# Optimization experiments

Measured on AMD Instinct MI355X. Metric: run time of the kernel, lower is better.

The kernel has to match this reference:

```python
import jax, jax.numpy as jnp
import numpy as np

N_NODES = 128
F = 64            # hidden channels (64x0e + 64x1o)
N_RBF = 8
H_R = 64          # radial MLP hidden
L = 2             # num_interactions
R_MAX = 5.0
AVG_NEIGH = 127.0
G_DIM = 16
N_SPECIES = 5

# static fully-connected edge list (no self edges): E = n*(n-1)
_idx = np.arange(N_NODES)
_s, _r = np.meshgrid(_idx, _idx, indexing='ij')
_mask = _s != _r
SENDERS = jnp.asarray(_s[_mask])    # [E]
RECEIVERS = jnp.asarray(_r[_mask])  # [E]


def setup_inputs() -> dict:
    key = jax.random.key(0)
    ks = jax.random.split(key, 12)
    inp = {
        'positions': jax.random.normal(ks[0], (32, N_NODES, 3), jnp.float32),
        'node_features': jax.random.randint(ks[1], (32, N_NODES), 0, N_SPECIES),
        'global_features': jax.random.normal(ks[2], (32, G_DIM), jnp.float32),
        # learned parameters
        'embed': jax.random.normal(ks[3], (N_SPECIES, F), jnp.float32) * 0.1,
        'glob_w': jax.random.normal(ks[4], (G_DIM, F), jnp.float32) * 0.1,
        'rbf_w1': jax.random.normal(ks[5], (L, N_RBF, H_R), jnp.float32) * 0.3,
        'rbf_b1': jnp.zeros((L, H_R), jnp.float32),
        'rbf_w2': jax.random.normal(ks[6], (L, H_R, 3 * F), jnp.float32) * 0.1,
        'ws': jax.random.normal(ks[7], (L, F, F), jnp.float32) * 0.1,
        'wv': jax.random.normal(ks[8], (L, F, F), jnp.float32) * 0.1,
        'wout': jax.random.normal(ks[9], (F,), jnp.float32) * 0.1,
        'final_scaling': jnp.ones((), jnp.float32),
    }
    return inp


def _rbf(d):
    # gaussian radial basis on [0, r_max]
    centers = jnp.linspace(0.0, R_MAX, N_RBF)
    width = R_MAX / N_RBF
    return jnp.exp(-((d[:, None] - centers) ** 2) / (2.0 * width * width))  # [E, N_RBF]


def _single(pos, species, glob, embed, glob_w, rbf_w1, rbf_b1, rbf_w2, ws, wv, wout, final_scaling):
    # graph construction + edge vectors
    edge_vec = pos[RECEIVERS] - pos[SENDERS]                 # [E,3]
    d = jnp.sqrt(jnp.sum(edge_vec ** 2, axis=-1) + 1e-12)   # [E]
    unit = edge_vec / d[:, None]                             # [E,3]
    phi = _rbf(d)                                            # [E,N_RBF]

    # node embedding (species one-hot lookup) conditioned on global features
    s = embed[species] + glob @ glob_w                       # [n,F] scalars
    v = jnp.zeros((N_NODES, F, 3), pos.dtype)                # [n,F,3] vectors

    for l in range(L):
        rw = jax.nn.silu(phi @ rbf_w1[l] + rbf_b1[l]) @ rbf_w2[l]  # [E,3F]
        r1, r2, r3 = jnp.split(rw, 3, axis=-1)               # each [E,F]
        ms = r1 * s[SENDERS]                                 # [E,F]
        mv = r2[..., None] * v[SENDERS] + (r3 * s[SENDERS])[..., None] * unit[:, None, :]  # [E,F,3]
        agg_s = jax.ops.segment_sum(ms, RECEIVERS, num_segments=N_NODES) / AVG_NEIGH
        agg_v = jax.ops.segment_sum(mv, RECEIVERS, num_segments=N_NODES) / AVG_NEIGH
        s = s + agg_s @ ws[l]
        v = v + jnp.einsum('nfd,fg->ngd', agg_v, wv[l])

    out = jnp.einsum('nfd,f->nd', v, wout)                   # equivariant readout [n,3]
    return (out - pos) * final_scaling


def reference(positions, node_features, global_features, embed, glob_w, rbf_w1,
              rbf_b1, rbf_w2, ws, wv, wout, final_scaling):
    fn = lambda p, sp, g: _single(p, sp, g, embed, glob_w, rbf_w1, rbf_b1,
                                  rbf_w2, ws, wv, wout, final_scaling)
    return jax.vmap(fn)(positions, node_features, global_features)
```

## Files before the change

### kernel.cpp

```cpp
#include <hip/hip_runtime.h>
#include <hip/hip_bf16.h>


#define NN 128
#define BB 32
#define FF 64

using f32x4  = __attribute__((ext_vector_type(4))) float;
using short8 = __attribute__((ext_vector_type(8))) short;
using half4  = __attribute__((ext_vector_type(4))) _Float16;

__device__ __forceinline__ unsigned short f2bf(float x) {
    unsigned int u = __float_as_uint(x);
    u += 0x7fff + ((u >> 16) & 1);
    return (unsigned short)(u >> 16);
}
__device__ __forceinline__ unsigned int f2bf_fast32(float x) {
    return (__float_as_uint(x) + 0x8000u) >> 16;
}

__global__ __launch_bounds__(256) void setup_kernel(
    const float* __restrict__ w2,
    const float* __restrict__ ws,
    const float* __restrict__ wv,
    const float* __restrict__ rbf_w1,
    const float* __restrict__ rbf_b1,
    const int* __restrict__ species, const float* __restrict__ glob,
    const float* __restrict__ embed, const float* __restrict__ glob_w,
    short* __restrict__ w2frag,
    float* __restrict__ wT4,
    _Float16* __restrict__ w1A,
    float* __restrict__ s)
{
    const int blk = blockIdx.x;
    if (blk < 192) {
        const int tid = blk * 256 + threadIdx.x;
        const int NFRAG = 24576;
        if (tid < NFRAG) {
            const int e  = tid & 7;
            const int l  = (tid >> 3) & 63;
            const int ks = (tid >> 9) & 1;
            const int q  = tid >> 10;
            const int nt = q % 3;
            const int wv_ = (q / 3) & 3;
            const int layer = q / 12;
            const int col = nt * 64 + wv_ * 16 + (l & 15);
            const int hb  = ks * 32 + (l >> 4) * 8 + e;
            const float val = w2[layer * 64 * 192 + hb * 192 + col] * (1.0f / 127.0f);
            w2frag[tid] = (short)f2bf(val);
        }
        const int tid2 = tid - NFRAG;
        if (tid2 >= 0 && tid2 < 16384) {
            const int c   = tid2 & 3;
            const int g   = (tid2 >> 2) & 63;
            const int ff4 = (tid2 >> 8) & 15;
            const int m   = (tid2 >> 12) & 1;
            const int layer = tid2 >> 13;
            const float* src = (m == 0 ? ws : wv) + layer * 4096;
            wT4[tid2] = src[(ff4 * 4 + c) * 64 + g];
        }
        const int tid3 = tid - NFRAG - 16384;
        if (tid3 >= 0 && tid3 < 2048) {
            const int e  = tid3 & 3;
            const int l  = (tid3 >> 2) & 63;
            const int wv_ = (tid3 >> 8) & 3;
            const int layer = tid3 >> 10;
            const int k = (l >> 4) * 4 + e;
            const int h = wv_ * 16 + (l & 15);
            float val = 0.0f;
            if (k < 8)       val = rbf_w1[layer * 512 + k * 64 + h];
            else if (k == 8) val = rbf_b1[layer * 64 + h];
            w1A[tid3] = (_Float16)val;
        }
    } else {
        const int node = (blk - 192) * 4 + (threadIdx.x >> 6);
        const int b = node >> 7;
        const int f = threadIdx.x & 63;
        const int sp = species[node];
        float acc = embed[sp * FF + f];
#pragma unroll
        for (int k = 0; k < 16; ++k)
            acc = fmaf(glob[b * 16 + k], glob_w[k * FF + f], acc);
        s[node * FF + f] = acc;
    }
}

template<int LAYER>
__global__ __launch_bounds__(256, 2) void msg_kernel(
    const float* __restrict__ pos,
    const float* __restrict__ s_in,
    const float* __restrict__ v_in,
    const half4* __restrict__ w1Abuf,
    const short* __restrict__ w2frag,
    const float* __restrict__ wT4,
    const float* __restrict__ wout,
    const float* __restrict__ scale,
    float* __restrict__ s_out,
    float* __restrict__ v_out,
    float* __restrict__ out)
{
    __shared__ unsigned short hid_lds[2 * NN * 64];
    __shared__ float4 unit_lds[2][NN];
    __shared__ __align__(16) char phi_pool[2 * NN * 32];

    const int blk = blockIdx.x;
    const int xcd = blk & 7;
    const int idx = blk >> 3;
    const int b = xcd * 4 + (idx >> 6);
    const int i0 = (idx & 63) * 2;

    const int t = threadIdx.x;
    const int w = t >> 6;
    const int l = t & 63;
    const float* pb = pos + b * NN * 3;

    const int f    = w * 16 + (l & 15);
    const int jsub = (l >> 4) * 4;
    const float* sb = s_in + b * NN * FF;
    const float4* vb4 = (LAYER > 0) ? ((const float4*)v_in) + b * NN * FF : nullptr;

    float sP[4]; float4 vP[4];
#pragma unroll
    for (int reg = 0; reg < 4; ++reg) {
        const int j = jsub + reg;
        sP[reg] = sb[j * FF + f];
        if (LAYER > 0) vP[reg] = vb4[j * FF + f];
    }

    short8 bfrag[3][2];
    {
        const short8* wf = (const short8*)w2frag;
#pragma unroll
        for (int nt = 0; nt < 3; ++nt) {
            if (LAYER == 0 && nt == 1) continue;
#pragma unroll
            for (int ks = 0; ks < 2; ++ks)
                bfrag[nt][ks] = wf[((w * 3 + nt) * 2 + ks) * 64 + l];
        }
    }

    {
        const int j = t & 127;
        const int rr = t >> 7;
        const int ie = i0 + rr;
        const float dx = pb[ie * 3 + 0] - pb[j * 3 + 0];
        const float dy = pb[ie * 3 + 1] - pb[j * 3 + 1];
        const float dz = pb[ie * 3 + 2] - pb[j * 3 + 2];
        const float d2 = fmaf(dx, dx, fmaf(dy, dy, fmaf(dz, dz, 1e-12f)));
        const float inv = __builtin_amdgcn_rsqf(d2);
        const float dd = d2 * inv;
        unit_lds[rr][j] = make_float4(dx * inv, dy * inv, dz * inv, 0.0f);
        const _Float16 zf = (_Float16)0.f;
        const half4 z4 = {zf, zf, zf, zf};
        half4 ph0, ph1;
#pragma unroll
        for (int r = 0; r < 4; ++r) {
            const float td0 = dd - (float)r * (5.0f / 7.0f);
            ph0[r] = (_Float16)__expf(td0 * td0 * -1.28f);
            const float td1 = dd - (float)(4 + r) * (5.0f / 7.0f);
            ph1[r] = (_Float16)__expf(td1 * td1 * -1.28f);
        }
        if (j == ie) { ph0 = z4; ph1 = z4; }
        char* rowp = phi_pool + rr * 4096 + j * 32;
        const int swz = ((j >> 2) & 3) << 3;
        *(half4*)(rowp + (0 ^ swz))  = ph0;
        *(half4*)(rowp + (8 ^ swz))  = ph1;
        half4 bias = {(j == ie) ? zf : (_Float16)1.0f, zf, zf, zf};
        *(half4*)(rowp + (16 ^ swz)) = bias;
        *(half4*)(rowp + (24 ^ swz)) = z4;
    }
    __syncthreads();

    {
        const half4 w1a = w1Abuf[w * 64 + l];
        const int jcol = l & 15;
        const int chunk = (l >> 4) * 8;
        const int hbyte = w * 32 + (l >> 4) * 8;
#pragma unroll
        for (int rr = 0; rr < 2; ++rr) {
            const char* phir = phi_pool + rr * 4096;
            char* hidr = (char*)hid_lds + rr * 16384;
#pragma unroll
            for (int mt = 0; mt < 8; ++mt) {
                const int j = mt * 16 + jcol;
                const half4 bphi = *(const half4*)(
                    phir + j * 32 + (chunk ^ (((j >> 2) & 3) << 3)));
                f32x4 pre = __builtin_amdgcn_mfma_f32_16x16x16f16(
                    w1a, bphi, (f32x4){0.f, 0.f, 0.f, 0.f}, 0, 0, 0);
                unsigned int pk[2];
#pragma unroll
                for (int p = 0; p < 2; ++p) {
                    float sv[2];
#pragma unroll
                    for (int q = 0; q < 2; ++q) {
                        const float z = pre[p * 2 + q];
                        const float ex = __expf(-z);
                        sv[q] = z * __builtin_amdgcn_rcpf(1.0f + ex);
                    }
                    pk[p] = f2bf_fast32(sv[0]) | (f2bf_fast32(sv[1]) << 16);
                }
                const int byte = j * 128 + (hbyte ^ ((j & 7) << 4));
                *(uint2*)(hidr + byte) = make_uint2(pk[0], pk[1]);
            }
        }
    }
    __syncthreads();

    float a0s = 0.f, a0x = 0.f, a0y = 0.f, a0z = 0.f;
    float a1s = 0.f, a1x = 0.f, a1y = 0.f, a1z = 0.f;

#pragma unroll
    for (int mt = 0; mt < 8; ++mt) {
        const int jA = mt * 16 + (l & 15);
        const int base = jA * 128;
        const int sw = (jA & 7) << 4;
        const int o0 = base + (((l >> 4) * 16 +  0) ^ sw);
        const int o1 = base + (((l >> 4) * 16 + 64) ^ sw);
        const char* hp = (const char*)hid_lds;
        const short8 a0r0 = *(const short8*)(hp + o0);
        const short8 a1r0 = *(const short8*)(hp + o1);
        const short8 a0r1 = *(const short8*)(hp + 16384 + o0);
        const short8 a1r1 = *(const short8*)(hp + 16384 + o1);

        f32x4 c0 = (f32x4){0.f, 0.f, 0.f, 0.f};
        f32x4 c1 = (f32x4){0.f, 0.f, 0.f, 0.f};
        f32x4 c2 = (f32x4){0.f, 0.f, 0.f, 0.f};
        c0 = __builtin_amdgcn_mfma_f32_16x16x32_bf16(a0r0, bfrag[0][0], c0, 0, 0, 0);
        c0 = __builtin_amdgcn_mfma_f32_16x16x32_bf16(a1r0, bfrag[0][1], c0, 0, 0, 0);
        if (LAYER > 0) {
            c1 = __builtin_amdgcn_mfma_f32_16x16x32_bf16(a0r0, bfrag[1][0], c1, 0, 0, 0);
            c1 = __builtin_amdgcn_mfma_f32_16x16x32_bf16(a1r0, bfrag[1][1], c1, 0, 0, 0);
        }
        c2 = __builtin_amdgcn_mfma_f32_16x16x32_bf16(a0r0, bfrag[2][0], c2, 0, 0, 0);
        c2 = __builtin_amdgcn_mfma_f32_16x16x32_bf16(a1r0, bfrag[2][1], c2, 0, 0, 0);

        float sN[4]; float4 vN[4];
        if (mt < 7) {
#pragma unroll
            for (int reg = 0; reg < 4; ++reg) {
                const int j = (mt + 1) * 16 + jsub + reg;
                sN[reg] = sb[j * FF + f];
                if (LAYER > 0) vN[reg] = vb4[j * FF + f];
            }
        }

#pragma unroll
        for (int reg = 0; reg < 4; ++reg) {
            const int j  = mt * 16 + jsub + reg;
            const float sj = sP[reg];
            const float r3s = c2[reg] * sj;
            const float4 u = unit_lds[0][j];
            a0s = fmaf(c0[reg], sj, a0s);
            a0x = fmaf(r3s, u.x, a0x);
            a0y = fmaf(r3s, u.y, a0y);
            a0z = fmaf(r3s, u.z, a0z);
            if (LAYER > 0) {
                a0x = fmaf(c1[reg], vP[reg].x, a0x);
                a0y = fmaf(c1[reg], vP[reg].y, a0y);
                a0z = fmaf(c1[reg], vP[reg].z, a0z);
            }
        }

        c0 = (f32x4){0.f, 0.f, 0.f, 0.f};
        c1 = (f32x4){0.f, 0.f, 0.f, 0.f};
        c2 = (f32x4){0.f, 0.f, 0.f, 0.f};
        c0 = __builtin_amdgcn_mfma_f32_16x16x32_bf16(a0r1, bfrag[0][0], c0, 0, 0, 0);
        c0 = __builtin_amdgcn_mfma_f32_16x16x32_bf16(a1r1, bfrag[0][1], c0, 0, 0, 0);
        if (LAYER > 0) {
            c1 = __builtin_amdgcn_mfma_f32_16x16x32_bf16(a0r1, bfrag[1][0], c1, 0, 0, 0);
            c1 = __builtin_amdgcn_mfma_f32_16x16x32_bf16(a1r1, bfrag[1][1], c1, 0, 0, 0);
        }
        c2 = __builtin_amdgcn_mfma_f32_16x16x32_bf16(a0r1, bfrag[2][0], c2, 0, 0, 0);
        c2 = __builtin_amdgcn_mfma_f32_16x16x32_bf16(a1r1, bfrag[2][1], c2, 0, 0, 0);

#pragma unroll
        for (int reg = 0; reg < 4; ++reg) {
            const int j  = mt * 16 + jsub + reg;
            const float sj = sP[reg];
            const float r3s = c2[reg] * sj;
            const float4 u = unit_lds[1][j];
            a1s = fmaf(c0[reg], sj, a1s);
            a1x = fmaf(r3s, u.x, a1x);
            a1y = fmaf(r3s, u.y, a1y);
            a1z = fmaf(r3s, u.z, a1z);
            if (LAYER > 0) {
                a1x = fmaf(c1[reg], vP[reg].x, a1x);
                a1y = fmaf(c1[reg], vP[reg].y, a1y);
                a1z = fmaf(c1[reg], vP[reg].z, a1z);
            }
        }

#pragma unroll
        for (int reg = 0; reg < 4; ++reg) {
            sP[reg] = sN[reg];
            if (LAYER > 0) vP[reg] = vN[reg];
        }
    }

    a0s += __shfl_xor(a0s, 16, 64); a0s += __shfl_xor(a0s, 32, 64);
    a0x += __shfl_xor(a0x, 16, 64); a0x += __shfl_xor(a0x, 32, 64);
    a0y += __shfl_xor(a0y, 16, 64); a0y += __shfl_xor(a0y, 32, 64);
    a0z += __shfl_xor(a0z, 16, 64); a0z += __shfl_xor(a0z, 32, 64);
    a1s += __shfl_xor(a1s, 16, 64); a1s += __shfl_xor(a1s, 32, 64);
    a1x += __shfl_xor(a1x, 16, 64); a1x += __shfl_xor(a1x, 32, 64);
    a1y += __shfl_xor(a1y, 16, 64); a1y += __shfl_xor(a1y, 32, 64);
    a1z += __shfl_xor(a1z, 16, 64); a1z += __shfl_xor(a1z, 32, 64);
    if (l < 16) {
        float* aggf = (float*)phi_pool;
        aggf[0 * 256 + 0 * 64 + f] = a0s;
        aggf[0 * 256 + 1 * 64 + f] = a0x;
        aggf[0 * 256 + 2 * 64 + f] = a0y;
        aggf[0 * 256 + 3 * 64 + f] = a0z;
        aggf[1 * 256 + 0 * 64 + f] = a1s;
        aggf[1 * 256 + 1 * 64 + f] = a1x;
        aggf[1 * 256 + 2 * 64 + f] = a1y;
        aggf[1 * 256 + 3 * 64 + f] = a1z;
    }
    __syncthreads();

    const int g = l;
    const int node0 = b * NN + i0;
    const int node1 = node0 + 1;
    const float4* wv4 = (const float4*)wT4;
    const float4* ag = (const float4*)phi_pool;
    if (LAYER == 0) {
        const int m = (w == 0) ? 0 : 1;
        const int row = (w == 0) ? 0 : w;
        float a0 = (w == 0) ? s_in[node0 * FF + g] : 0.0f;
        float a1 = (w == 0) ? s_in[node1 * FF + g] : 0.0f;
#pragma unroll
        for (int k = 0; k < 16; ++k) {
            const float4 w4 = wv4[(m * 16 + k) * 64 + g];
            const float4 x0 = ag[0 * 64 + row * 16 + k];
            const float4 x1 = ag[1 * 64 + row * 16 + k];
            a0 = fmaf(x0.x, w4.x, a0); a0 = fmaf(x0.y, w4.y, a0);
            a0 = fmaf(x0.z, w4.z, a0); a0 = fmaf(x0.w, w4.w, a0);
            a1 = fmaf(x1.x, w4.x, a1); a1 = fmaf(x1.y, w4.y, a1);
            a1 = fmaf(x1.z, w4.z, a1); a1 = fmaf(x1.w, w4.w, a1);
        }
        if (w == 0) {
            s_out[node0 * FF + g] = a0;
            s_out[node1 * FF + g] = a1;
        } else {
            v_out[(node0 * FF + g) * 4 + (w - 1)] = a0;
            v_out[(node1 * FF + g) * 4 + (w - 1)] = a1;
        }
    } else {
        if (w > 0) {
            const int d = w - 1;
            float a0 = v_in[(node0 * FF + g) * 4 + d];
            float a1 = v_in[(node1 * FF + g) * 4 + d];
#pragma unroll
            for (int k = 0; k < 16; ++k) {
                const float4 w4 = wv4[(16 + k) * 64 + g];
                const float4 x0 = ag[0 * 64 + w * 16 + k];
                const float4 x1 = ag[1 * 64 + w * 16 + k];
                a0 = fmaf(x0.x, w4.x, a0); a0 = fmaf(x0.y, w4.y, a0);
                a0 = fmaf(x0.z, w4.z, a0); a0 = fmaf(x0.w, w4.w, a0);
                a1 = fmaf(x1.x, w4.x, a1); a1 = fmaf(x1.y, w4.y, a1);
                a1 = fmaf(x1.z, w4.z, a1); a1 = fmaf(x1.w, w4.w, a1);
            }
            const float wg = wout[g];
            float p0 = a0 * wg;
            float p1 = a1 * wg;
#pragma unroll
            for (int off = 1; off < 64; off <<= 1) {
                p0 += __shfl_xor(p0, off, 64);
                p1 += __shfl_xor(p1, off, 64);
            }
            if (l == 0) {
                const float sc = scale[0];
                out[node0 * 3 + d] = (p0 - pos[node0 * 3 + d]) * sc;
                out[node1 * 3 + d] = (p1 - pos[node1 * 3 + d]) * sc;
            }
        }
    }
}

extern "C" void kernel_launch(void* const* d_in, const int* in_sizes, int n_in,
                              void* d_out, int out_size, void* d_ws, size_t ws_size,
                              hipStream_t stream) {
    const float* pos     = (const float*)d_in[0];
    const int*   species = (const int*)  d_in[1];
    const float* glob    = (const float*)d_in[2];
    const float* embed   = (const float*)d_in[3];
    const float* glob_w  = (const float*)d_in[4];
    const float* rbf_w1  = (const float*)d_in[5];
    const float* rbf_b1  = (const float*)d_in[6];
    const float* rbf_w2  = (const float*)d_in[7];
    const float* ws      = (const float*)d_in[8];
    const float* wv      = (const float*)d_in[9];
    const float* wout    = (const float*)d_in[10];
    const float* scale   = (const float*)d_in[11];

    float* wsf = (float*)d_ws;
    float* s0     = wsf;
    float* s1     = wsf + 262144;
    float* v1     = wsf + 524288;
    short* w2frag = (short*)(wsf + 1572864);
    float* wT4    = wsf + 1585152;
    _Float16* w1A = (_Float16*)(wsf + 1601536);
    float* outp = (float*)d_out;

    setup_kernel<<<dim3(192 + BB * NN / 4), 256, 0, stream>>>(
        rbf_w2, ws, wv, rbf_w1, rbf_b1, species, glob, embed, glob_w,
        w2frag, wT4, w1A, s0);

    msg_kernel<0><<<dim3(NN * BB / 2), 256, 0, stream>>>(
        pos, s0, nullptr,
        (const half4*)w1A, w2frag, wT4, wout, scale,
        s1, v1, nullptr);

    msg_kernel<1><<<dim3(NN * BB / 2), 256, 0, stream>>>(
        pos, s1, v1,
        (const half4*)(w1A + 1024), w2frag + 12288, wT4 + 8192, wout, scale,
        nullptr, nullptr, outp);
}
```

Measured before the change: 67.72 us.

## Process four receiver nodes per block to amortize weight fragment loads

Each message block now handles four receivers instead of two, looping twice over the existing two-receiver pipeline and staging the per-receiver aggregates in a dedicated shared buffer. The radial weight fragments and first-layer weights are loaded once per block and reused across both passes, and the final node-update matmul reuses each weight load across four nodes. The grid is halved to 1024 blocks, which lowers parallelism and adds an extra barrier per pass. Shared memory also grows slightly, which may affect occupancy.

Measured after the change: 75.50 us. 11.5% more time.

```diff
diff --git a/kernel.cpp b/kernel.cpp
--- a/kernel.cpp
+++ b/kernel.cpp
@@ -102,12 +102,13 @@
     __shared__ unsigned short hid_lds[2 * NN * 64];
     __shared__ float4 unit_lds[2][NN];
     __shared__ __align__(16) char phi_pool[2 * NN * 32];
+    __shared__ __align__(16) float aggL[4][4][64];
 
     const int blk = blockIdx.x;
     const int xcd = blk & 7;
     const int idx = blk >> 3;
-    const int b = xcd * 4 + (idx >> 6);
-    const int i0 = (idx & 63) * 2;
+    const int b = xcd * 4 + (idx >> 5);
+    const int iq = (idx & 31) * 4;
 
     const int t = threadIdx.x;
     const int w = t >> 6;
@@ -119,14 +120,6 @@
     const float* sb = s_in + b * NN * FF;
     const float4* vb4 = (LAYER > 0) ? ((const float4*)v_in) + b * NN * FF : nullptr;
 
-    float sP[4]; float4 vP[4];
-#pragma unroll
-    for (int reg = 0; reg < 4; ++reg) {
-        const int j = jsub + reg;
-        sP[reg] = sb[j * FF + f];
-        if (LAYER > 0) vP[reg] = vb4[j * FF + f];
-    }
-
     short8 bfrag[3][2];
     {
         const short8* wf = (const short8*)w2frag;
@@ -138,240 +131,254 @@
                 bfrag[nt][ks] = wf[((w * 3 + nt) * 2 + ks) * 64 + l];
         }
     }
-
-    {
-        const int j = t & 127;
-        const int rr = t >> 7;
-        const int ie = i0 + rr;
-        const float dx = pb[ie * 3 + 0] - pb[j * 3 + 0];
-        const float dy = pb[ie * 3 + 1] - pb[j * 3 + 1];
-        const float dz = pb[ie * 3 + 2] - pb[j * 3 + 2];
-        const float d2 = fmaf(dx, dx, fmaf(dy, dy, fmaf(dz, dz, 1e-12f)));
-        const float inv = __builtin_amdgcn_rsqf(d2);
-        const float dd = d2 * inv;
-        unit_lds[rr][j] = make_float4(dx * inv, dy * inv, dz * inv, 0.0f);
-        const _Float16 zf = (_Float16)0.f;
-        const half4 z4 = {zf, zf, zf, zf};
-        half4 ph0, ph1;
-#pragma unroll
-        for (int r = 0; r < 4; ++r) {
-            const float td0 = dd - (float)r * (5.0f / 7.0f);
-            ph0[r] = (_Float16)__expf(td0 * td0 * -1.28f);
-            const float td1 = dd - (float)(4 + r) * (5.0f / 7.0f);
-            ph1[r] = (_Float16)__expf(td1 * td1 * -1.28f);
-        }
-        if (j == ie) { ph0 = z4; ph1 = z4; }
-        char* rowp = phi_pool + rr * 4096 + j * 32;
-        const int swz = ((j >> 2) & 3) << 3;
-        *(half4*)(rowp + (0 ^ swz))  = ph0;
-        *(half4*)(rowp + (8 ^ swz))  = ph1;
-        half4 bias = {(j == ie) ? zf : (_Float16)1.0f, zf, zf, zf};
-        *(half4*)(rowp + (16 ^ swz)) = bias;
-        *(half4*)(rowp + (24 ^ swz)) = z4;
+    const half4 w1a = w1Abuf[w * 64 + l];
+
+    for (int p = 0; p < 2; ++p) {
+        const int i0 = iq + 2 * p;
+
+        {
+            const int j = t & 127;
+            const int rr = t >> 7;
+            const int ie = i0 + rr;
+            const float dx = pb[ie * 3 + 0] - pb[j * 3 + 0];
+            const float dy = pb[ie * 3 + 1] - pb[j * 3 + 1];
+            const float dz = pb[ie * 3 + 2] - pb[j * 3 + 2];
+            const float d2 = fmaf(dx, dx, fmaf(dy, dy, fmaf(dz, dz, 1e-12f)));
+            const float inv = __builtin_amdgcn_rsqf(d2);
+            const float dd = d2 * inv;
+            unit_lds[rr][j] = make_float4(dx * inv, dy * inv, dz * inv, 0.0f);
+            const _Float16 zf = (_Float16)0.f;
+            const half4 z4 = {zf, zf, zf, zf};
+            half4 ph0, ph1;
+#pragma unroll
+            for (int r = 0; r < 4; ++r) {
+                const float td0 = dd - (float)r * (5.0f / 7.0f);
+                ph0[r] = (_Float16)__expf(td0 * td0 * -1.28f);
+                const float td1 = dd - (float)(4 + r) * (5.0f / 7.0f);
+                ph1[r] = (_Float16)__expf(td1 * td1 * -1.28f);
+            }
+            if (j == ie) { ph0 = z4; ph1 = z4; }
+            char* rowp = phi_pool + rr * 4096 + j * 32;
+            const int swz = ((j >> 2) & 3) << 3;
+            *(half4*)(rowp + (0 ^ swz))  = ph0;
+            *(half4*)(rowp + (8 ^ swz))  = ph1;
+            half4 bias = {(j == ie) ? zf : (_Float16)1.0f, zf, zf, zf};
+            *(half4*)(rowp + (16 ^ swz)) = bias;
+            *(half4*)(rowp + (24 ^ swz)) = z4;
+        }
+        __syncthreads();
+
+        {
+            const int jcol = l & 15;
+            const int chunk = (l >> 4) * 8;
+            const int hbyte = w * 32 + (l >> 4) * 8;
+#pragma unroll
+            for (int rr = 0; rr < 2; ++rr) {
+                const char* phir = phi_pool + rr * 4096;
+                char* hidr = (char*)hid_lds + rr * 16384;
+#pragma unroll
+                for (int mt = 0; mt < 8; ++mt) {
+                    const int j = mt * 16 + jcol;
+                    const half4 bphi = *(const half4*)(
+                        phir + j * 32 + (chunk ^ (((j >> 2) & 3) << 3)));
+                    f32x4 pre = __builtin_amdgcn_mfma_f32_16x16x16f16(
+                        w1a, bphi, (f32x4){0.f, 0.f, 0.f, 0.f}, 0, 0, 0);
+                    unsigned int pk[2];
+#pragma unroll
+                    for (int pp = 0; pp < 2; ++pp) {
+                        float sv[2];
+#pragma unroll
+                        for (int q = 0; q < 2; ++q) {
+                            const float z = pre[pp * 2 + q];
+                            const float ex = __expf(-z);
+                            sv[q] = z * __builtin_amdgcn_rcpf(1.0f + ex);
+                        }
+                        pk[pp] = f2bf_fast32(sv[0]) | (f2bf_fast32(sv[1]) << 16);
+                    }
+                    const int byte = j * 128 + (hbyte ^ ((j & 7) << 4));
+                    *(uint2*)(hidr + byte) = make_uint2(pk[0], pk[1]);
+                }
+            }
+        }
+        __syncthreads();
+
+        float a0s = 0.f, a0x = 0.f, a0y = 0.f, a0z = 0.f;
+        float a1s = 0.f, a1x = 0.f, a1y = 0.f, a1z = 0.f;
+
+        float sP[4]; float4 vP[4];
+#pragma unroll
+        for (int reg = 0; reg < 4; ++reg) {
+            const int j = jsub + reg;
+            sP[reg] = sb[j * FF + f];
+            if (LAYER > 0) vP[reg] = vb4[j * FF + f];
+        }
+
+#pragma unroll
+        for (int mt = 0; mt < 8; ++mt) {
+            const int jA = mt * 16 + (l & 15);
+            const int base = jA * 128;
+            const int sw = (jA & 7) << 4;
+            const int o0 = base + (((l >> 4) * 16 +  0) ^ sw);
+            const int o1 = base + (((l >> 4) * 16 + 64) ^ sw);
+            const char* hp = (const char*)hid_lds;
+            const short8 a0r0 = *(const short8*)(hp + o0);
+            const short8 a1r0 = *(const short8*)(hp + o1);
+            const short8 a0r1 = *(const short8*)(hp + 16384 + o0);
+            const short8 a1r1 = *(const short8*)(hp + 16384 + o1);
+
+            f32x4 c0 = (f32x4){0.f, 0.f, 0.f, 0.f};
+            f32x4 c1 = (f32x4){0.f, 0.f, 0.f, 0.f};
+            f32x4 c2 = (f32x4){0.f, 0.f, 0.f, 0.f};
+            c0 = __builtin_amdgcn_mfma_f32_16x16x32_bf16(a0r0, bfrag[0][0], c0, 0, 0, 0);
+            c0 = __builtin_amdgcn_mfma_f32_16x16x32_bf16(a1r0, bfrag[0][1], c0, 0, 0, 0);
+            if (LAYER > 0) {
+                c1 = __builtin_amdgcn_mfma_f32_16x16x32_bf16(a0r0, bfrag[1][0], c1, 0, 0, 0);
+                c1 = __builtin_amdgcn_mfma_f32_16x16x32_bf16(a1r0, bfrag[1][1], c1, 0, 0, 0);
+            }
+            c2 = __builtin_amdgcn_mfma_f32_16x16x32_bf16(a0r0, bfrag[2][0], c2, 0, 0, 0);
+            c2 = __builtin_amdgcn_mfma_f32_16x16x32_bf16(a1r0, bfrag[2][1], c2, 0, 0, 0);
+
+            float sN[4]; float4 vN[4];
+            if (mt < 7) {
+#pragma unroll
+                for (int reg = 0; reg < 4; ++reg) {
+                    const int j = (mt + 1) * 16 + jsub + reg;
+                    sN[reg] = sb[j * FF + f];
+                    if (LAYER > 0) vN[reg] = vb4[j * FF + f];
+                }
+            }
+
+#pragma unroll
+            for (int reg = 0; reg < 4; ++reg) {
+                const int j  = mt * 16 + jsub + reg;
+                const float sj = sP[reg];
+                const float r3s = c2[reg] * sj;
+                const float4 u = unit_lds[0][j];
+                a0s = fmaf(c0[reg], sj, a0s);
+                a0x = fmaf(r3s, u.x, a0x);
+                a0y = fmaf(r3s, u.y, a0y);
+                a0z = fmaf(r3s, u.z, a0z);
+                if (LAYER > 0) {
+                    a0x = fmaf(c1[reg], vP[reg].x, a0x);
+                    a0y = fmaf(c1[reg], vP[reg].y, a0y);
+                    a0z = fmaf(c1[reg], vP[reg].z, a0z);
+                }
+            }
+
+            c0 = (f32x4){0.f, 0.f, 0.f, 0.f};
+            c1 = (f32x4){0.f, 0.f, 0.f, 0.f};
+            c2 = (f32x4){0.f, 0.f, 0.f, 0.f};
+            c0 = __builtin_amdgcn_mfma_f32_16x16x32_bf16(a0r1, bfrag[0][0], c0, 0, 0, 0);
+            c0 = __builtin_amdgcn_mfma_f32_16x16x32_bf16(a1r1, bfrag[0][1], c0, 0, 0, 0);
+            if (LAYER > 0) {
+                c1 = __builtin_amdgcn_mfma_f32_16x16x32_bf16(a0r1, bfrag[1][0], c1, 0, 0, 0);
+                c1 = __builtin_amdgcn_mfma_f32_16x16x32_bf16(a1r1, bfrag[1][1], c1, 0, 0, 0);
+            }
+            c2 = __builtin_amdgcn_mfma_f32_16x16x32_bf16(a0r1, bfrag[2][0], c2, 0, 0, 0);
+            c2 = __builtin_amdgcn_mfma_f32_16x16x32_bf16(a1r1, bfrag[2][1], c2, 0, 0, 0);
+
+#pragma unroll
+            for (int reg = 0; reg < 4; ++reg) {
+                const int j  = mt * 16 + jsub + reg;
+                const float sj = sP[reg];
+                const float r3s = c2[reg] * sj;
+                const float4 u = unit_lds[1][j];
+                a1s = fmaf(c0[reg], sj, a1s);
+                a1x = fmaf(r3s, u.x, a1x);
+                a1y = fmaf(r3s, u.y, a1y);
+                a1z = fmaf(r3s, u.z, a1z);
+                if (LAYER > 0) {
+                    a1x = fmaf(c1[reg], vP[reg].x, a1x);
+                    a1y = fmaf(c1[reg], vP[reg].y, a1y);
+                    a1z = fmaf(c1[reg], vP[reg].z, a1z);
+                }
+            }
+
+#pragma unroll
+            for (int reg = 0; reg < 4; ++reg) {
+                sP[reg] = sN[reg];
+                if (LAYER > 0) vP[reg] = vN[reg];
+            }
+        }
+
+        a0s += __shfl_xor(a0s, 16, 64); a0s += __shfl_xor(a0s, 32, 64);
+        a0x += __shfl_xor(a0x, 16, 64); a0x += __shfl_xor(a0x, 32, 64);
+        a0y += __shfl_xor(a0y, 16, 64); a0y += __shfl_xor(a0y, 32, 64);
+        a0z += __shfl_xor(a0z, 16, 64); a0z += __shfl_xor(a0z, 32, 64);
+        a1s += __shfl_xor(a1s, 16, 64); a1s += __shfl_xor(a1s, 32, 64);
+        a1x += __shfl_xor(a1x, 16, 64); a1x += __shfl_xor(a1x, 32, 64);
+        a1y += __shfl_xor(a1y, 16, 64); a1y += __shfl_xor(a1y, 32, 64);
+        a1z += __shfl_xor(a1z, 16, 64); a1z += __shfl_xor(a1z, 32, 64);
+        if (l < 16) {
+            const int r0 = 2 * p;
+            aggL[r0][0][f] = a0s;  aggL[r0][1][f] = a0x;
+            aggL[r0][2][f] = a0y;  aggL[r0][3][f] = a0z;
+            aggL[r0 + 1][0][f] = a1s;  aggL[r0 + 1][1][f] = a1x;
+            aggL[r0 + 1][2][f] = a1y;  aggL[r0 + 1][3][f] = a1z;
+        }
+        __syncthreads();
     }
-    __syncthreads();
-
-    {
-        const half4 w1a = w1Abuf[w * 64 + l];
-        const int jcol = l & 15;
-        const int chunk = (l >> 4) * 8;
-        const int hbyte = w * 32 + (l >> 4) * 8;
-#pragma unroll
-        for (int rr = 0; rr < 2; ++rr) {
-            const char* phir = phi_pool + rr * 4096;
-            char* hidr = (char*)hid_lds + rr * 16384;
-#pragma unroll
-            for (int mt = 0; mt < 8; ++mt) {
-                const int j = mt * 16 + jcol;
-                const half4 bphi = *(const half4*)(
-                    phir + j * 32 + (chunk ^ (((j >> 2) & 3) << 3)));
-                f32x4 pre = __builtin_amdgcn_mfma_f32_16x16x16f16(
-                    w1a, bphi, (f32x4){0.f, 0.f, 0.f, 0.f}, 0, 0, 0);
-                unsigned int pk[2];
-#pragma unroll
-                for (int p = 0; p < 2; ++p) {
-                    float sv[2];
-#pragma unroll
-                    for (int q = 0; q < 2; ++q) {
-                        const float z = pre[p * 2 + q];
-                        const float ex = __expf(-z);
-                        sv[q] = z * __builtin_amdgcn_rcpf(1.0f + ex);
-                    }
-                    pk[p] = f2bf_fast32(sv[0]) | (f2bf_fast32(sv[1]) << 16);
-                }
-                const int byte = j * 128 + (hbyte ^ ((j & 7) << 4));
-                *(uint2*)(hidr + byte) = make_uint2(pk[0], pk[1]);
-            }
-        }
-    }
-    __syncthreads();
-
-    float a0s = 0.f, a0x = 0.f, a0y = 0.f, a0z = 0.f;
-    float a1s = 0.f, a1x = 0.f, a1y = 0.f, a1z = 0.f;
-
-#pragma unroll
-    for (int mt = 0; mt < 8; ++mt) {
-        const int jA = mt * 16 + (l & 15);
-        const int base = jA * 128;
-        const int sw = (jA & 7) << 4;
-        const int o0 = base + (((l >> 4) * 16 +  0) ^ sw);
-        const int o1 = base + (((l >> 4) * 16 + 64) ^ sw);
-        const char* hp = (const char*)hid_lds;
-        const short8 a0r0 = *(const short8*)(hp + o0);
-        const short8 a1r0 = *(const short8*)(hp + o1);
-        const short8 a0r1 = *(const short8*)(hp + 16384 + o0);
-        const short8 a1r1 = *(const short8*)(hp + 16384 + o1);
-
-        f32x4 c0 = (f32x4){0.f, 0.f, 0.f, 0.f};
-        f32x4 c1 = (f32x4){0.f, 0.f, 0.f, 0.f};
-        f32x4 c2 = (f32x4){0.f, 0.f, 0.f, 0.f};
-        c0 = __builtin_amdgcn_mfma_f32_16x16x32_bf16(a0r0, bfrag[0][0], c0, 0, 0, 0);
-        c0 = __builtin_amdgcn_mfma_f32_16x16x32_bf16(a1r0, bfrag[0][1], c0, 0, 0, 0);
-        if (LAYER > 0) {
-            c1 = __builtin_amdgcn_mfma_f32_16x16x32_bf16(a0r0, bfrag[1][0], c1, 0, 0, 0);
-            c1 = __builtin_amdgcn_mfma_f32_16x16x32_bf16(a1r0, bfrag[1][1], c1, 0, 0, 0);
-        }
-        c2 = __builtin_amdgcn_mfma_f32_16x16x32_bf16(a0r0, bfrag[2][0], c2, 0, 0, 0);
-        c2 = __builtin_amdgcn_mfma_f32_16x16x32_bf16(a1r0, bfrag[2][1], c2, 0, 0, 0);
-
-        float sN[4]; float4 vN[4];
-        if (mt < 7) {
-#pragma unroll
-            for (int reg = 0; reg < 4; ++reg) {
-                const int j = (mt + 1) * 16 + jsub + reg;
-                sN[reg] = sb[j * FF + f];
-                if (LAYER > 0) vN[reg] = vb4[j * FF + f];
-            }
-        }
-
-#pragma unroll
-        for (int reg = 0; reg < 4; ++reg) {
-            const int j  = mt * 16 + jsub + reg;
-            const float sj = sP[reg];
-            const float r3s = c2[reg] * sj;
-            const float4 u = unit_lds[0][j];
-            a0s = fmaf(c0[reg], sj, a0s);
-            a0x = fmaf(r3s, u.x, a0x);
-            a0y = fmaf(r3s, u.y, a0y);
-            a0z = fmaf(r3s, u.z, a0z);
-            if (LAYER > 0) {
-                a0x = fmaf(c1[reg], vP[reg].x, a0x);
-                a0y = fmaf(c1[reg], vP[reg].y, a0y);
-                a0z = fmaf(c1[reg], vP[reg].z, a0z);
-            }
-        }
-
-        c0 = (f32x4){0.f, 0.f, 0.f, 0.f};
-        c1 = (f32x4){0.f, 0.f, 0.f, 0.f};
-        c2 = (f32x4){0.f, 0.f, 0.f, 0.f};
-        c0 = __builtin_amdgcn_mfma_f32_16x16x32_bf16(a0r1, bfrag[0][0], c0, 0, 0, 0);
-        c0 = __builtin_amdgcn_mfma_f32_16x16x32_bf16(a1r1, bfrag[0][1], c0, 0, 0, 0);
-        if (LAYER > 0) {
-            c1 = __builtin_amdgcn_mfma_f32_16x16x32_bf16(a0r1, bfrag[1][0], c1, 0, 0, 0);
-            c1 = __builtin_amdgcn_mfma_f32_16x16x32_bf16(a1r1, bfrag[1][1], c1, 0, 0, 0);
-        }
-        c2 = __builtin_amdgcn_mfma_f32_16x16x32_bf16(a0r1, bfrag[2][0], c2, 0, 0, 0);
-        c2 = __builtin_amdgcn_mfma_f32_16x16x32_bf16(a1r1, bfrag[2][1], c2, 0, 0, 0);
-
-#pragma unroll
-        for (int reg = 0; reg < 4; ++reg) {
-            const int j  = mt * 16 + jsub + reg;
-            const float sj = sP[reg];
-            const float r3s = c2[reg] * sj;
-            const float4 u = unit_lds[1][j];
-            a1s = fmaf(c0[reg], sj, a1s);
-            a1x = fmaf(r3s, u.x, a1x);
-            a1y = fmaf(r3s, u.y, a1y);
-            a1z = fmaf(r3s, u.z, a1z);
-            if (LAYER > 0) {
-                a1x = fmaf(c1[reg], vP[reg].x, a1x);
-                a1y = fmaf(c1[reg], vP[reg].y, a1y);
-                a1z = fmaf(c1[reg], vP[reg].z, a1z);
-            }
-        }
-
-#pragma unroll
-        for (int reg = 0; reg < 4; ++reg) {
-            sP[reg] = sN[reg];
-            if (LAYER > 0) vP[reg] = vN[reg];
-        }
-    }
-
-    a0s += __shfl_xor(a0s, 16, 64); a0s += __shfl_xor(a0s, 32, 64);
-    a0x += __shfl_xor(a0x, 16, 64); a0x += __shfl_xor(a0x, 32, 64);
-    a0y += __shfl_xor(a0y, 16, 64); a0y += __shfl_xor(a0y, 32, 64);
-    a0z += __shfl_xor(a0z, 16, 64); a0z += __shfl_xor(a0z, 32, 64);
-    a1s += __shfl_xor(a1s, 16, 64); a1s += __shfl_xor(a1s, 32, 64);
-    a1x += __shfl_xor(a1x, 16, 64); a1x += __shfl_xor(a1x, 32, 64);
-    a1y += __shfl_xor(a1y, 16, 64); a1y += __shfl_xor(a1y, 32, 64);
-    a1z += __shfl_xor(a1z, 16, 64); a1z += __shfl_xor(a1z, 32, 64);
-    if (l < 16) {
-        float* aggf = (float*)phi_pool;
-        aggf[0 * 256 + 0 * 64 + f] = a0s;
-        aggf[0 * 256 + 1 * 64 + f] = a0x;
-        aggf[0 * 256 + 2 * 64 + f] = a0y;
-        aggf[0 * 256 + 3 * 64 + f] = a0z;
-        aggf[1 * 256 + 0 * 64 + f] = a1s;
-        aggf[1 * 256 + 1 * 64 + f] = a1x;
-        aggf[1 * 256 + 2 * 64 + f] = a1y;
-        aggf[1 * 256 + 3 * 64 + f] = a1z;
-    }
-    __syncthreads();
 
     const int g = l;
-    const int node0 = b * NN + i0;
-    const int node1 = node0 + 1;
+    const int node0 = b * NN + iq;
     const float4* wv4 = (const float4*)wT4;
-    const float4* ag = (const float4*)phi_pool;
+    const float4 (*ag)[4][16] = (const float4(*)[4][16])aggL;
     if (LAYER == 0) {
         const int m = (w == 0) ? 0 : 1;
         const int row = (w == 0) ? 0 : w;
-        float a0 = (w == 0) ? s_in[node0 * FF + g] : 0.0f;
-        float a1 = (w == 0) ? s_in[node1 * FF + g] : 0.0f;
+        float a[4];
+#pragma unroll
+        for (int r = 0; r < 4; ++r)
+            a[r] = (w == 0) ? s_in[(node0 + r) * FF + g] : 0.0f;
 #pragma unroll
         for (int k = 0; k < 16; ++k) {
             const float4 w4 = wv4[(m * 16 + k) * 64 + g];
-            const float4 x0 = ag[0 * 64 + row * 16 + k];
-            const float4 x1 = ag[1 * 64 + row * 16 + k];
-            a0 = fmaf(x0.x, w4.x, a0); a0 = fmaf(x0.y, w4.y, a0);
-            a0 = fmaf(x0.z, w4.z, a0); a0 = fmaf(x0.w, w4.w, a0);
-            a1 = fmaf(x1.x, w4.x, a1); a1 = fmaf(x1.y, w4.y, a1);
-            a1 = fmaf(x1.z, w4.z, a1); a1 = fmaf(x1.w, w4.w, a1);
-        }
-        if (w == 0) {
-            s_out[node0 * FF + g] = a0;
-            s_out[node1 * FF + g] = a1;
-        } else {
-            v_out[(node0 * FF + g) * 4 + (w - 1)] = a0;
-            v_out[(node1 * FF + g) * 4 + (w - 1)] = a1;
+#pragma unroll
+            for (int r = 0; r < 4; ++r) {
+                const float4 x = ag[r][row][k];
+                a[r] = fmaf(x.x, w4.x, a[r]); a[r] = fmaf(x.y, w4.y, a[r]);
+                a[r] = fmaf(x.z, w4.z, a[r]); a[r] = fmaf(x.w, w4.w, a[r]);
+            }
+        }
+#pragma unroll
+        for (int r = 0; r < 4; ++r) {
+            if (w == 0) s_out[(node0 + r) * FF + g] = a[r];
+            else        v_out[((node0 + r) * FF + g) * 4 + (w - 1)] = a[r];
         }
     } else {
         if (w > 0) {
             const int d = w - 1;
-            float a0 = v_in[(node0 * FF + g) * 4 + d];
-            float a1 = v_in[(node1 * FF + g) * 4 + d];
+            float a[4];
+#pragma unroll
+            for (int r = 0; r < 4; ++r)
+                a[r] = v_in[((node0 + r) * FF + g) * 4 + d];
 #pragma unroll
             for (int k = 0; k < 16; ++k) {
                 const float4 w4 = wv4[(16 + k) * 64 + g];
-                const float4 x0 = ag[0 * 64 + w * 16 + k];
-                const float4 x1 = ag[1 * 64 + w * 16 + k];
-                a0 = fmaf(x0.x, w4.x, a0); a0 = fmaf(x0.y, w4.y, a0);
-                a0 = fmaf(x0.z, w4.z, a0); a0 = fmaf(x0.w, w4.w, a0);
-                a1 = fmaf(x1.x, w4.x, a1); a1 = fmaf(x1.y, w4.y, a1);
-                a1 = fmaf(x1.z, w4.z, a1); a1 = fmaf(x1.w, w4.w, a1);
+#pragma unroll
+                for (int r = 0; r < 4; ++r) {
+                    const float4 x = ag[r][w][k];
+                    a[r] = fmaf(x.x, w4.x, a[r]); a[r] = fmaf(x.y, w4.y, a[r]);
+                    a[r] = fmaf(x.z, w4.z, a[r]); a[r] = fmaf(x.w, w4.w, a[r]);
+                }
             }
             const float wg = wout[g];
-            float p0 = a0 * wg;
-            float p1 = a1 * wg;
+            float pr[4];
+#pragma unroll
+            for (int r = 0; r < 4; ++r) pr[r] = a[r] * wg;
 #pragma unroll
             for (int off = 1; off < 64; off <<= 1) {
-                p0 += __shfl_xor(p0, off, 64);
-                p1 += __shfl_xor(p1, off, 64);
+#pragma unroll
+                for (int r = 0; r < 4; ++r)
+                    pr[r] += __shfl_xor(pr[r], off, 64);
             }
             if (l == 0) {
                 const float sc = scale[0];
-                out[node0 * 3 + d] = (p0 - pos[node0 * 3 + d]) * sc;
-                out[node1 * 3 + d] = (p1 - pos[node1 * 3 + d]) * sc;
+#pragma unroll
+                for (int r = 0; r < 4; ++r) {
+                    const int node = node0 + r;
+                    out[node * 3 + d] = (pr[r] - pos[node * 3 + d]) * sc;
+                }
             }
         }
     }
@@ -406,12 +413,12 @@
         rbf_w2, ws, wv, rbf_w1, rbf_b1, species, glob, embed, glob_w,
         w2frag, wT4, w1A, s0);
 
-    msg_kernel<0><<<dim3(NN * BB / 2), 256, 0, stream>>>(
+    msg_kernel<0><<<dim3(NN * BB / 4), 256, 0, stream>>>(
         pos, s0, nullptr,
         (const half4*)w1A, w2frag, wT4, wout, scale,
         s1, v1, nullptr);
 
-    msg_kernel<1><<<dim3(NN * BB / 2), 256, 0, stream>>>(
+    msg_kernel<1><<<dim3(NN * BB / 4), 256, 0, stream>>>(
         pos, s1, v1,
         (const half4*)(w1A + 1024), w2frag + 12288, wT4 + 8192, wout, scale,
         nullptr, nullptr, outp);
```
